# Kernel optimization log

Measured on AMD Instinct MI355X. Metric: run time of the kernel, lower is better.

Reference implementation:

```python
import jax, jax.numpy as jnp
import numpy as np

N = 20000      # nodes
E = 320000     # edges (avg degree 16)
IN, HID, OUT, H = 128, 32, 32, 8
NEG_SLOPE = 0.2


def _gat_conv(x, src, dst, W, al, ar, b):
    """One DGL-style GATConv. x: [N, F_in], W: [F_in, H*D], al/ar: [H, D], b: [H*D].
    Returns [N, H, D]."""
    n = x.shape[0]
    Hh, D = al.shape
    feat = (x @ W).reshape(n, Hh, D)                      # [N,H,D]
    el = jnp.sum(feat * al[None], axis=-1)                # [N,H]
    er = jnp.sum(feat * ar[None], axis=-1)                # [N,H]
    e = jax.nn.leaky_relu(el[src] + er[dst], NEG_SLOPE)   # [E,H]
    # edge softmax over incoming edges of each dst node (stable)
    emax = jax.ops.segment_max(e, dst, num_segments=n)    # [N,H]
    ee = jnp.exp(e - emax[dst])                           # [E,H]
    denom = jax.ops.segment_sum(ee, dst, num_segments=n)  # [N,H]
    alpha = ee / denom[dst]                               # [E,H]
    msg = feat[src] * alpha[:, :, None]                   # [E,H,D] gather+weight
    out = jax.ops.segment_sum(msg, dst, num_segments=n)   # [N,H,D] scatter-add
    return out + b.reshape(1, Hh, D)


def setup_inputs() -> dict:
    key = jax.random.key(0)
    ks = jax.random.split(key, 11)
    return {
        "x":   jax.random.normal(ks[0], (N, IN), dtype=jnp.float32),
        "src": jax.random.randint(ks[1], (E,), 0, N, dtype=jnp.int32),
        "dst": jax.random.randint(ks[2], (E,), 0, N, dtype=jnp.int32),
        "W1":  jax.random.normal(ks[3], (IN, H * HID), dtype=jnp.float32) * 0.1,
        "al1": jax.random.normal(ks[4], (H, HID), dtype=jnp.float32) * 0.1,
        "ar1": jax.random.normal(ks[5], (H, HID), dtype=jnp.float32) * 0.1,
        "b1":  jnp.zeros((H * HID,), dtype=jnp.float32),
        "W2":  jax.random.normal(ks[6], (HID, H * OUT), dtype=jnp.float32) * 0.1,
        "al2": jax.random.normal(ks[7], (H, OUT), dtype=jnp.float32) * 0.1,
        "ar2": jax.random.normal(ks[8], (H, OUT), dtype=jnp.float32) * 0.1,
        "b2":  jnp.zeros((H * OUT,), dtype=jnp.float32),
    }


def reference(x, src, dst, W1, al1, ar1, b1, W2, al2, ar2, b2):
    h = _gat_conv(x, src, dst, W1, al1, ar1, b1)          # [N,H,HID]
    h = jnp.mean(jax.nn.relu(h), axis=1)                  # [N,HID]
    h = _gat_conv(h, src, dst, W2, al2, ar2, b2)          # [N,H,OUT]
    return jnp.mean(h, axis=1)                            # [N,OUT]
```

## Files before the change

### kernel.cpp

```cpp
#include <hip/hip_runtime.h>
#include <hip/hip_bf16.h>

#define N_NODES 20000
#define N_EDGES 320000
#define F_IN    128
#define F_HID   32
#define NHEAD   8
#define FDIM    256
#define CAP     96

typedef __hip_bfloat16 bf16;
typedef __attribute__((ext_vector_type(8))) short short8;
typedef __attribute__((ext_vector_type(4))) float f32x4;

__device__ __forceinline__ unsigned short f2bf_rne(float f){
  unsigned u = __float_as_uint(f);
  unsigned r = u + 0x7FFFu + ((u >> 16) & 1u);
  return (unsigned short)(r >> 16);
}
__device__ __forceinline__ float bf2f(unsigned short s){
  return __uint_as_float((unsigned)s << 16);
}

#define ZB ((N_NODES + 255) / 256)
__global__ void init_kernel(const float* __restrict__ W1, const float* __restrict__ W2,
                            const float* __restrict__ al2, const float* __restrict__ ar2,
                            int* __restrict__ cnt,
                            unsigned short* __restrict__ h1, unsigned short* __restrict__ l1,
                            float* __restrict__ q_lt, float* __restrict__ q_rt){
  const int b = blockIdx.x;
  if (b < ZB){
    int i = b*256 + threadIdx.x;
    if (i < N_NODES) cnt[i] = 0;
  } else if (b < ZB + 128){
    int i = (b - ZB)*256 + threadIdx.x;
    int n = i >> 7, k = i & 127;
    float v = W1[(size_t)k*FDIM + n];
    unsigned short hs = f2bf_rne(v);
    h1[i] = hs;
    l1[i] = f2bf_rne(v - bf2f(hs));
  } else {
    int t = threadIdx.x;
    int k = t >> 3, hh = t & 7;
    float sl = 0.f, sr = 0.f;
    #pragma unroll
    for (int d = 0; d < 32; d++){
      float w = W2[(size_t)k*FDIM + hh*32 + d];
      sl = fmaf(w, al2[hh*32 + d], sl);
      sr = fmaf(w, ar2[hh*32 + d], sr);
    }
    q_lt[t] = sl;
    q_rt[t] = sr;
  }
}

#define FILLB  ((N_EDGES + 255) / 256)
#define GEMMB  (N_NODES / 16)
__global__ __launch_bounds__(256) void scatter_gemm_kernel(
    const int* __restrict__ src, const int* __restrict__ dst,
    int* __restrict__ cnt, int* __restrict__ bucket,
    const float* __restrict__ X,
    const unsigned short* __restrict__ Wthi, const unsigned short* __restrict__ Wtlo,
    const float* __restrict__ al, const float* __restrict__ ar,
    unsigned short* __restrict__ feat, float* __restrict__ el, float* __restrict__ er)
{
  const int b = blockIdx.x;
  if (b < FILLB){
    int i = b*256 + threadIdx.x;
    if (i < N_EDGES){
      int d = dst[i];
      int p = atomicAdd(&cnt[d], 1);
      if (p < CAP) bucket[(size_t)d*CAP + p] = src[i];
    }
    return;
  }

  constexpr int K = F_IN;
  const int tid  = threadIdx.x;
  const int wv   = tid >> 6;
  const int lane = tid & 63;
  const int quad = lane >> 4;
  const int l16  = lane & 15;
  const int m0   = (b - FILLB) * 16;
  constexpr int NC = K / 32;

  short8 Ah[NC], Al_[NC];
  {
    const float* xrow = X + (size_t)(m0 + l16)*K;
    #pragma unroll
    for (int c = 0; c < NC; c++){
      float4 a0 = *(const float4*)(xrow + c*32 + quad*8);
      float4 a1 = *(const float4*)(xrow + c*32 + quad*8 + 4);
      const float vs[8] = {a0.x,a0.y,a0.z,a0.w,a1.x,a1.y,a1.z,a1.w};
      #pragma unroll
      for (int j = 0; j < 8; j++){
        unsigned short hs = f2bf_rne(vs[j]);
        Ah[c][j]  = (short)hs;
        Al_[c][j] = (short)f2bf_rne(vs[j] - bf2f(hs));
      }
    }
  }

  float elp[8], erp[8];
  #pragma unroll
  for (int j = 0; j < 8; j++){ elp[j] = 0.f; erp[j] = 0.f; }

  #pragma unroll
  for (int t = 0; t < 4; t++){
    const int nc = wv*64 + t*16;
    const size_t brow = (size_t)(nc + l16) * K;
    f32x4 acc = {0.f, 0.f, 0.f, 0.f};
    #pragma unroll
    for (int c = 0; c < NC; c++){
      short8 Bh = *(const short8*)(Wthi + brow + c*32 + quad*8);
      short8 Bl = *(const short8*)(Wtlo + brow + c*32 + quad*8);
      acc = __builtin_amdgcn_mfma_f32_16x16x32_bf16(Ah[c],  Bh, acc, 0, 0, 0);
      acc = __builtin_amdgcn_mfma_f32_16x16x32_bf16(Ah[c],  Bl, acc, 0, 0, 0);
      acc = __builtin_amdgcn_mfma_f32_16x16x32_bf16(Al_[c], Bh, acc, 0, 0, 0);
    }
    const float alv = al[nc + l16];
    const float arv = ar[nc + l16];
    const int hl = t >> 1;
    #pragma unroll
    for (int r = 0; r < 4; r++){
      float v = acc[r];
      feat[(size_t)(m0 + quad*4 + r)*FDIM + nc + l16] = f2bf_rne(v);
      elp[r*2 + hl] = fmaf(v, alv, elp[r*2 + hl]);
      erp[r*2 + hl] = fmaf(v, arv, erp[r*2 + hl]);
    }
  }

  #pragma unroll
  for (int off = 1; off <= 8; off <<= 1){
    #pragma unroll
    for (int j = 0; j < 8; j++){
      elp[j] += __shfl_xor(elp[j], off);
      erp[j] += __shfl_xor(erp[j], off);
    }
  }
  __shared__ float el_lds[16][8], er_lds[16][8];
  if (l16 == 0){
    #pragma unroll
    for (int r = 0; r < 4; r++){
      #pragma unroll
      for (int hl = 0; hl < 2; hl++){
        el_lds[quad*4 + r][wv*2 + hl] = elp[r*2 + hl];
        er_lds[quad*4 + r][wv*2 + hl] = erp[r*2 + hl];
      }
    }
  }
  __syncthreads();
  if (tid < 128){
    int row = tid >> 3, h = tid & 7;
    el[(size_t)(m0 + row)*NHEAD + h] = el_lds[row][h];
    er[(size_t)(m0 + row)*NHEAD + h] = er_lds[row][h];
  }
}

__global__ __launch_bounds__(256) void edge_agg_l1(
    const bf16* __restrict__ feat, const float* __restrict__ el,
    const float* __restrict__ er, const int* __restrict__ cnt,
    const int* __restrict__ bucket, const float* __restrict__ bias,
    const float* __restrict__ q_lt, const float* __restrict__ q_rt,
    unsigned short* __restrict__ h_out, float* __restrict__ el2,
    float* __restrict__ er2)
{
  const int tid  = threadIdx.x;
  const int wv   = tid >> 6;
  const int lane = tid & 63;
  const int n    = blockIdx.x*4 + wv;

  __shared__ float t_all[4][CAP*9];
  __shared__ int   s_all[4][CAP];
  __shared__ float sum_all[4][NHEAD];
  __shared__ float v_all[4][256];
  float* t_w = t_all[wv];
  int*   s_w = s_all[wv];

  int C = cnt[n];
  if (C > CAP) C = CAP;

  const float4* er4 = (const float4*)(er + (size_t)n*NHEAD);
  float4 era = er4[0], erb = er4[1];
  const float erv[8] = {era.x, era.y, era.z, era.w, erb.x, erb.y, erb.z, erb.w};

  for (int idx = lane; idx < C*2; idx += 64){
    const int e = idx >> 1, j = idx & 1;
    const int sidx = bucket[(size_t)n*CAP + e];
    if (j == 0) s_w[e] = sidx;
    float4 a = ((const float4*)(el + (size_t)sidx*NHEAD))[j];
    const float ev[4] = {a.x, a.y, a.z, a.w};
    #pragma unroll
    for (int hh = 0; hh < 4; hh++){
      float v = ev[hh] + erv[j*4 + hh];
      t_w[e*9 + j*4 + hh] = (v > 0.f) ? v : 0.2f*v;
    }
  }
  {
    const int h = lane >> 3, d = lane & 7;
    float lm = -INFINITY;
    for (int e = d; e < C; e += 8) lm = fmaxf(lm, t_w[e*9 + h]);
    #pragma unroll
    for (int off = 4; off >= 1; off >>= 1) lm = fmaxf(lm, __shfl_xor(lm, off));
    float ls = 0.f;
    for (int e = d; e < C; e += 8){
      float ex = __expf(t_w[e*9 + h] - lm);
      t_w[e*9 + h] = ex;
      ls += ex;
    }
    #pragma unroll
    for (int off = 4; off >= 1; off >>= 1) ls += __shfl_xor(ls, off);
    if (d == 0) sum_all[wv][h] = ls;
  }

  const int sub = lane >> 5;
  const int l   = lane & 31;
  const int hB  = l >> 2;
  const int coff = l << 3;
  float acc[8] = {0,0,0,0,0,0,0,0};
  int e = sub;
  float4 fv;
  if (e < C) fv = *(const float4*)(feat + (size_t)s_w[e]*FDIM + coff);
  while (e < C){
    const int en = e + 2;
    float4 fnext;
    if (en < C) fnext = *(const float4*)(feat + (size_t)s_w[en]*FDIM + coff);
    const float w = t_w[e*9 + hB];
    const unsigned* u = (const unsigned*)&fv;
    #pragma unroll
    for (int j = 0; j < 4; j++){
      float flo = __uint_as_float(u[j] << 16);
      float fhi = __uint_as_float(u[j] & 0xFFFF0000u);
      acc[2*j]   = fmaf(w, flo, acc[2*j]);
      acc[2*j+1] = fmaf(w, fhi, acc[2*j+1]);
    }
    fv = fnext;
    e = en;
  }
  #pragma unroll
  for (int j = 0; j < 8; j++) acc[j] += __shfl_xor(acc[j], 32);

  if (lane < 32){
    const float s = sum_all[wv][l >> 2];
    const float4* b4 = (const float4*)(bias + coff);
    float4 ba = b4[0], bb = b4[1];
    float bv[8] = {ba.x, ba.y, ba.z, ba.w, bb.x, bb.y, bb.z, bb.w};
    float v[8];
    #pragma unroll
    for (int j = 0; j < 8; j++){
      float val = (C > 0) ? (acc[j] / s) : 0.f;
      val += bv[j];
      val = fmaxf(val, 0.f);
      v[j] = val;
    }
    float4* v4 = (float4*)&v_all[wv][coff];
    v4[0] = make_float4(v[0], v[1], v[2], v[3]);
    v4[1] = make_float4(v[4], v[5], v[6], v[7]);
  }
  if (lane < 32){
    float hsum = 0.f;
    #pragma unroll
    for (int hh = 0; hh < 8; hh++) hsum += v_all[wv][hh*32 + lane];
    hsum *= 0.125f;
    h_out[(size_t)n*32 + lane] = f2bf_rne(hsum);

    float4 qa0 = ((const float4*)(q_lt + lane*8))[0];
    float4 qa1 = ((const float4*)(q_lt + lane*8))[1];
    float4 qb0 = ((const float4*)(q_rt + lane*8))[0];
    float4 qb1 = ((const float4*)(q_rt + lane*8))[1];
    float pl[8] = {hsum*qa0.x, hsum*qa0.y, hsum*qa0.z, hsum*qa0.w,
                   hsum*qa1.x, hsum*qa1.y, hsum*qa1.z, hsum*qa1.w};
    float pr[8] = {hsum*qb0.x, hsum*qb0.y, hsum*qb0.z, hsum*qb0.w,
                   hsum*qb1.x, hsum*qb1.y, hsum*qb1.z, hsum*qb1.w};
    #pragma unroll
    for (int off = 1; off <= 16; off <<= 1){
      #pragma unroll
      for (int j = 0; j < 8; j++){
        pl[j] += __shfl_xor(pl[j], off);
        pr[j] += __shfl_xor(pr[j], off);
      }
    }
    if (l == 0){
      #pragma unroll
      for (int j = 0; j < 8; j++){
        el2[(size_t)n*NHEAD + j] = pl[j];
        er2[(size_t)n*NHEAD + j] = pr[j];
      }
    }
  }
}

__global__ __launch_bounds__(256) void edge_agg_l2(
    const unsigned short* __restrict__ h_bf, const float* __restrict__ el2,
    const float* __restrict__ er2, const int* __restrict__ cnt,
    const int* __restrict__ bucket, const float* __restrict__ W2,
    const float* __restrict__ b2, float* __restrict__ outp)
{
  const int tid  = threadIdx.x;
  const int wv   = tid >> 6;
  const int lane = tid & 63;
  const int n    = blockIdx.x*4 + wv;

  __shared__ float t_all[4][CAP*9];
  __shared__ int   s_all[4][CAP];
  __shared__ float sum_all[4][NHEAD];
  __shared__ float A_lds[4][NHEAD][33];
  __shared__ float red[4][256];
  float* t_w = t_all[wv];
  int*   s_w = s_all[wv];

  int C = cnt[n];
  if (C > CAP) C = CAP;

  const float4* er4 = (const float4*)(er2 + (size_t)n*NHEAD);
  float4 era = er4[0], erb = er4[1];
  const float erv[8] = {era.x, era.y, era.z, era.w, erb.x, erb.y, erb.z, erb.w};

  for (int idx = lane; idx < C*2; idx += 64){
    const int e = idx >> 1, j = idx & 1;
    const int sidx = bucket[(size_t)n*CAP + e];
    if (j == 0) s_w[e] = sidx;
    float4 a = ((const float4*)(el2 + (size_t)sidx*NHEAD))[j];
    const float ev[4] = {a.x, a.y, a.z, a.w};
    #pragma unroll
    for (int hh = 0; hh < 4; hh++){
      float v = ev[hh] + erv[j*4 + hh];
      t_w[e*9 + j*4 + hh] = (v > 0.f) ? v : 0.2f*v;
    }
  }
  {
    const int h = lane >> 3, d = lane & 7;
    float lm = -INFINITY;
    for (int e = d; e < C; e += 8) lm = fmaxf(lm, t_w[e*9 + h]);
    #pragma unroll
    for (int off = 4; off >= 1; off >>= 1) lm = fmaxf(lm, __shfl_xor(lm, off));
    float ls = 0.f;
    for (int e = d; e < C; e += 8){
      float ex = __expf(t_w[e*9 + h] - lm);
      t_w[e*9 + h] = ex;
      ls += ex;
    }
    #pragma unroll
    for (int off = 4; off >= 1; off >>= 1) ls += __shfl_xor(ls, off);
    if (d == 0) sum_all[wv][h] = ls;
  }

  const int h  = lane & 7;
  const int dg = lane >> 3;
  float A0=0.f, A1=0.f, A2=0.f, A3=0.f;
  int e = 0;
  ushort4 hv;
  if (e < C) hv = *(const ushort4*)(h_bf + (size_t)s_w[e]*32 + dg*4);
  while (e < C){
    const int en = e + 1;
    ushort4 hnext;
    if (en < C) hnext = *(const ushort4*)(h_bf + (size_t)s_w[en]*32 + dg*4);
    const float w = t_w[e*9 + h];
    A0 = fmaf(w, bf2f(hv.x), A0);
    A1 = fmaf(w, bf2f(hv.y), A1);
    A2 = fmaf(w, bf2f(hv.z), A2);
    A3 = fmaf(w, bf2f(hv.w), A3);
    hv = hnext;
    e = en;
  }
  {
    const float s = sum_all[wv][h];
    const float inv = (C > 0) ? (1.f / s) : 0.f;
    A_lds[wv][h][dg*4 + 0] = A0 * inv;
    A_lds[wv][h][dg*4 + 1] = A1 * inv;
    A_lds[wv][h][dg*4 + 2] = A2 * inv;
    A_lds[wv][h][dg*4 + 3] = A3 * inv;
  }
  __syncthreads();

  {
    const int c  = tid;
    const int hc = c >> 5;
    float p0=0.f, p1=0.f, p2=0.f, p3=0.f;
    for (int k = 0; k < F_HID; k++){
      float w = W2[(size_t)k*FDIM + c];
      p0 = fmaf(A_lds[0][hc][k], w, p0);
      p1 = fmaf(A_lds[1][hc][k], w, p1);
      p2 = fmaf(A_lds[2][hc][k], w, p2);
      p3 = fmaf(A_lds[3][hc][k], w, p3);
    }
    red[0][c] = p0; red[1][c] = p1; red[2][c] = p2; red[3][c] = p3;
  }
  __syncthreads();
  if (tid < 128){
    const int nn = tid >> 5, d = tid & 31;
    float s = 0.f, bm = 0.f;
    #pragma unroll
    for (int hh = 0; hh < 8; hh++){
      s  += red[nn][hh*32 + d];
      bm += b2[hh*32 + d];
    }
    outp[(size_t)(blockIdx.x*4 + nn)*32 + d] = (s + bm) * 0.125f;
  }
}

extern "C" void kernel_launch(void* const* d_in, const int* in_sizes, int n_in,
                              void* d_out, int out_size, void* d_ws, size_t ws_size,
                              hipStream_t stream)
{
  const float* x   = (const float*)d_in[0];
  const int*   src = (const int*)  d_in[1];
  const int*   dst = (const int*)  d_in[2];
  const float* W1  = (const float*)d_in[3];
  const float* al1 = (const float*)d_in[4];
  const float* ar1 = (const float*)d_in[5];
  const float* b1  = (const float*)d_in[6];
  const float* W2  = (const float*)d_in[7];
  const float* al2 = (const float*)d_in[8];
  const float* ar2 = (const float*)d_in[9];
  const float* b2  = (const float*)d_in[10];
  (void)in_sizes; (void)n_in; (void)out_size; (void)ws_size;

  size_t o = 0;
  char* base = (char*)d_ws;
  auto take = [&](size_t bytes) -> char* {
    char* p = base + o;
    o += (bytes + 255) & ~(size_t)255;
    return p;
  };
  unsigned short* feat  = (unsigned short*)take((size_t)N_NODES*FDIM*2);
  float* el1    = (float*)take((size_t)N_NODES*NHEAD*4);
  float* er1    = (float*)take((size_t)N_NODES*NHEAD*4);
  float* el2    = (float*)take((size_t)N_NODES*NHEAD*4);
  float* er2    = (float*)take((size_t)N_NODES*NHEAD*4);
  int*   cnt    = (int*)  take((size_t)N_NODES*4);
  int*   bucket = (int*)  take((size_t)N_NODES*CAP*4);
  unsigned short* hbf  = (unsigned short*)take((size_t)N_NODES*F_HID*2);
  unsigned short* W1th = (unsigned short*)take((size_t)FDIM*F_IN*2);
  unsigned short* W1tl = (unsigned short*)take((size_t)FDIM*F_IN*2);
  float* q_lt   = (float*)take((size_t)F_HID*NHEAD*4);
  float* q_rt   = (float*)take((size_t)F_HID*NHEAD*4);

  init_kernel<<<ZB + 129, 256, 0, stream>>>(
      W1, W2, al2, ar2, cnt, W1th, W1tl, q_lt, q_rt);

  scatter_gemm_kernel<<<FILLB + GEMMB, 256, 0, stream>>>(
      src, dst, cnt, bucket, x, W1th, W1tl, al1, ar1, feat, el1, er1);

  edge_agg_l1<<<N_NODES/4, 256, 0, stream>>>(
      (const bf16*)feat, el1, er1, cnt, bucket, b1, q_lt, q_rt, hbf, el2, er2);

  edge_agg_l2<<<N_NODES/4, 256, 0, stream>>>(
      hbf, el2, er2, cnt, bucket, W2, b2, (float*)d_out);
}
```

Baseline: 193.3 us.

## Replace per-edge global atomic bucketing with two-pass LDS-binned bucket build

The single-pass CSR-like bucket fill, which did one global atomic per edge on a per-node counter, is replaced by two passes. The first bins edges into 64-node groups, using shared-memory histograms and one global atomic per group per block, and writes packed (local dst, src) records. A new kernel then builds each group's per-node buckets in LDS and writes them out with coalesced int4 stores. The aim is to cut global atomic contention and scattered writes, at the cost of an extra launch, an intermediate record buffer, and a 16-bit src packing that only holds because N is below 65536.

```diff
diff --git a/kernel.cpp b/kernel.cpp
--- a/kernel.cpp
+++ b/kernel.cpp
@@ -9,6 +9,11 @@
 #define FDIM    256
 #define CAP     96
 
+#define GROUPS  313
+#define GCAP    2048
+#define EPB     2048
+#define P1B     ((N_EDGES + EPB - 1) / EPB)
+
 typedef __hip_bfloat16 bf16;
 typedef __attribute__((ext_vector_type(8))) short short8;
 typedef __attribute__((ext_vector_type(4))) float f32x4;
@@ -22,18 +27,16 @@
   return __uint_as_float((unsigned)s << 16);
 }
 
-#define ZB ((N_NODES + 255) / 256)
 __global__ void init_kernel(const float* __restrict__ W1, const float* __restrict__ W2,
                             const float* __restrict__ al2, const float* __restrict__ ar2,
-                            int* __restrict__ cnt,
+                            int* __restrict__ gcnt,
                             unsigned short* __restrict__ h1, unsigned short* __restrict__ l1,
                             float* __restrict__ q_lt, float* __restrict__ q_rt){
   const int b = blockIdx.x;
-  if (b < ZB){
-    int i = b*256 + threadIdx.x;
-    if (i < N_NODES) cnt[i] = 0;
-  } else if (b < ZB + 128){
-    int i = (b - ZB)*256 + threadIdx.x;
+  if (b == 0){
+    for (int i = threadIdx.x; i < GROUPS; i += 256) gcnt[i] = 0;
+  } else if (b < 129){
+    int i = (b - 1)*256 + threadIdx.x;
     int n = i >> 7, k = i & 127;
     float v = W1[(size_t)k*FDIM + n];
     unsigned short hs = f2bf_rne(v);
@@ -54,34 +57,59 @@
   }
 }
 
-#define FILLB  ((N_EDGES + 255) / 256)
 #define GEMMB  (N_NODES / 16)
-__global__ __launch_bounds__(256) void scatter_gemm_kernel(
+__global__ __launch_bounds__(256) void gemm_p1_kernel(
     const int* __restrict__ src, const int* __restrict__ dst,
-    int* __restrict__ cnt, int* __restrict__ bucket,
+    int* __restrict__ gcnt, unsigned* __restrict__ recs,
     const float* __restrict__ X,
     const unsigned short* __restrict__ Wthi, const unsigned short* __restrict__ Wtlo,
     const float* __restrict__ al, const float* __restrict__ ar,
     unsigned short* __restrict__ feat, float* __restrict__ el, float* __restrict__ er)
 {
   const int b = blockIdx.x;
-  if (b < FILLB){
-    int i = b*256 + threadIdx.x;
-    if (i < N_EDGES){
-      int d = dst[i];
-      int p = atomicAdd(&cnt[d], 1);
-      if (p < CAP) bucket[(size_t)d*CAP + p] = src[i];
+  const int tid = threadIdx.x;
+
+  if (b < P1B){
+    __shared__ int hist[GROUPS];
+    for (int t = tid; t < GROUPS; t += 256) hist[t] = 0;
+    __syncthreads();
+
+    unsigned rec[8]; int bin[8]; bool val[8];
+    const int e0 = b * EPB;
+    #pragma unroll
+    for (int k = 0; k < 8; k++){
+      int i = e0 + k*256 + tid;
+      val[k] = (i < N_EDGES);
+      if (val[k]){
+        int s = src[i];
+        int d = dst[i];
+        bin[k] = d >> 6;
+        rec[k] = (unsigned)(((d & 63) << 16) | s);
+        atomicAdd(&hist[bin[k]], 1);
+      }
+    }
+    __syncthreads();
+    for (int t = tid; t < GROUPS; t += 256){
+      int h = hist[t];
+      hist[t] = (h > 0) ? atomicAdd(&gcnt[t], h) : 0;
+    }
+    __syncthreads();
+    #pragma unroll
+    for (int k = 0; k < 8; k++){
+      if (val[k]){
+        int pos = atomicAdd(&hist[bin[k]], 1);
+        if (pos < GCAP) recs[(size_t)bin[k]*GCAP + pos] = rec[k];
+      }
     }
     return;
   }
 
   constexpr int K = F_IN;
-  const int tid  = threadIdx.x;
   const int wv   = tid >> 6;
   const int lane = tid & 63;
   const int quad = lane >> 4;
   const int l16  = lane & 15;
-  const int m0   = (b - FILLB) * 16;
+  const int m0   = (b - P1B) * 16;
   constexpr int NC = K / 32;
 
   short8 Ah[NC], Al_[NC];
@@ -155,6 +183,34 @@
     el[(size_t)(m0 + row)*NHEAD + h] = el_lds[row][h];
     er[(size_t)(m0 + row)*NHEAD + h] = er_lds[row][h];
   }
+}
+
+__global__ __launch_bounds__(256) void bucket_build_kernel(
+    const unsigned* __restrict__ recs, const int* __restrict__ gcnt,
+    int* __restrict__ cnt, int* __restrict__ bucket)
+{
+  const int g  = blockIdx.x;
+  const int n0 = g << 6;
+  __shared__ int lcnt[64];
+  __shared__ int lbuck[64*CAP];
+  if (threadIdx.x < 64) lcnt[threadIdx.x] = 0;
+  __syncthreads();
+
+  int m = gcnt[g]; if (m > GCAP) m = GCAP;
+  for (int r = threadIdx.x; r < m; r += 256){
+    unsigned w = recs[(size_t)g*GCAP + r];
+    int d = (int)(w >> 16);
+    int p = atomicAdd(&lcnt[d], 1);
+    if (p < CAP) lbuck[d*CAP + p] = (int)(w & 0xFFFFu);
+  }
+  __syncthreads();
+
+  int nn = N_NODES - n0; if (nn > 64) nn = 64;
+  if (threadIdx.x < nn) cnt[n0 + threadIdx.x] = lcnt[threadIdx.x];
+  const int tot4 = (nn * CAP) >> 2;
+  int4* gb = (int4*)(bucket + (size_t)n0 * CAP);
+  const int4* lb = (const int4*)lbuck;
+  for (int i = threadIdx.x; i < tot4; i += 256) gb[i] = lb[i];
 }
 
 __global__ __launch_bounds__(256) void edge_agg_l1(
@@ -435,12 +491,16 @@
   unsigned short* W1tl = (unsigned short*)take((size_t)FDIM*F_IN*2);
   float* q_lt   = (float*)take((size_t)F_HID*NHEAD*4);
   float* q_rt   = (float*)take((size_t)F_HID*NHEAD*4);
-
-  init_kernel<<<ZB + 129, 256, 0, stream>>>(
-      W1, W2, al2, ar2, cnt, W1th, W1tl, q_lt, q_rt);
-
-  scatter_gemm_kernel<<<FILLB + GEMMB, 256, 0, stream>>>(
-      src, dst, cnt, bucket, x, W1th, W1tl, al1, ar1, feat, el1, er1);
+  int*   gcnt   = (int*)  take((size_t)GROUPS*4);
+  unsigned* recs = (unsigned*)take((size_t)GROUPS*GCAP*4);
+
+  init_kernel<<<130, 256, 0, stream>>>(
+      W1, W2, al2, ar2, gcnt, W1th, W1tl, q_lt, q_rt);
+
+  gemm_p1_kernel<<<P1B + GEMMB, 256, 0, stream>>>(
+      src, dst, gcnt, recs, x, W1th, W1tl, al1, ar1, feat, el1, er1);
+
+  bucket_build_kernel<<<GROUPS, 256, 0, stream>>>(recs, gcnt, cnt, bucket);
 
   edge_agg_l1<<<N_NODES/4, 256, 0, stream>>>(
       (const bf16*)feat, el1, er1, cnt, bucket, b1, q_lt, q_rt, hbf, el2, er2);
```

New measurement: 187.8 us. -2.9%, faster.
